# Performance work log

Measured on AMD Instinct MI355X. Metric: run time of the kernel, lower is better.

The kernel has to match this reference:

```python
import jax, jax.numpy as jnp
import numpy as np

B, T, F, C, D, R = 8, 1000, 96, 16, 64, 4
S = F // R
EPS = 1e-5


def _ln(x, g, b):
    # LayerNorm over last (frequency) dim, matching nn.LayerNorm(fe) on [B,C,T,F]
    m = jnp.mean(x, -1, keepdims=True)
    v = jnp.mean((x - m) ** 2, -1, keepdims=True)
    return (x - m) / jnp.sqrt(v + EPS) * g + b


def _gelu(x):
    return jax.nn.gelu(x, approximate=False)  # torch nn.GELU default (erf)


def setup_inputs() -> dict:
    key = jax.random.key(0)
    ks = jax.random.split(key, 16)
    def nrm(k, shape, fan_in):
        return jax.random.normal(k, shape, jnp.float32) / np.sqrt(fan_in)
    return {
        "input": jax.random.normal(ks[0], (B, 2, T, F), jnp.float32),
        "ln_in_g": jnp.ones((F,), jnp.float32),
        "ln_in_b": jnp.zeros((F,), jnp.float32),
        "w_in": nrm(ks[1], (C, 2), 2),
        "b_in": jnp.zeros((C,), jnp.float32),
        "gru_wx": nrm(ks[2], (3 * C, C), C),   # z|r|n input projections (1x1 conv, no bias)
        "gru_wh": nrm(ks[3], (3 * C, C), C),   # z|r|n hidden projections
        "ln_att_g": jnp.ones((F,), jnp.float32),
        "ln_att_b": jnp.zeros((F,), jnp.float32),
        "wq": nrm(ks[4], (D, C), C),
        "bq": jnp.zeros((D,), jnp.float32),
        "wk": nrm(ks[5], (D, C), C),
        "bk": jnp.zeros((D,), jnp.float32),
        "wv": nrm(ks[6], (D, C), C),
        "bv": jnp.zeros((D,), jnp.float32),
        "wo": nrm(ks[7], (C, D), D),
        "bo": jnp.zeros((C,), jnp.float32),
        "ln_m_g": jnp.ones((F,), jnp.float32),
        "ln_m_b": jnp.zeros((F,), jnp.float32),
        "w_m1": nrm(ks[8], (C, C), C),
        "b_m1": jnp.zeros((C,), jnp.float32),
        "w_m2": nrm(ks[9], (C, C), C),
        "b_m2": jnp.zeros((C,), jnp.float32),
        "ln_out_g": jnp.ones((F,), jnp.float32),
        "ln_out_b": jnp.zeros((F,), jnp.float32),
        "w_out": nrm(ks[10], (2, C), C),
        "b_out": jnp.zeros((2,), jnp.float32),
    }


def _fwd(input, ln_in_g, ln_in_b, w_in, b_in, gru_wx, gru_wh,
         ln_att_g, ln_att_b, wq, bq, wk, bk, wv, bv, wo, bo,
         ln_m_g, ln_m_b, w_m1, b_m1, w_m2, b_m2,
         ln_out_g, ln_out_b, w_out, b_out):
    b = input.shape[0]
    # conv_in: LayerNorm -> 1x1 Conv (2->C) -> GELU
    x = _gelu(jnp.einsum('oc,bctf->botf', w_in, _ln(input, ln_in_g, ln_in_b))
              + b_in[None, :, None, None])  # [B,C,T,F]

    # ConvGRU (kernel 1, no bias): precompute input gates, scan over time
    gx = jnp.einsum('gc,bctf->tbgf', gru_wx, x)  # [T,B,3C,F]
    h0 = jnp.zeros((b, C, F), x.dtype)

    def step(h, gx_t):
        gh = jnp.einsum('gc,bcf->bgf', gru_wh, h)
        zx, rx, nx = jnp.split(gx_t, 3, axis=1)
        zh, rh, nh = jnp.split(gh, 3, axis=1)
        z = jax.nn.sigmoid(zx + zh)
        r = jax.nn.sigmoid(rx + rh)
        n = jnp.tanh(nx + r * nh)
        h = (1.0 - z) * n + z * h
        return h, h

    h_last, hs = jax.lax.scan(step, h0, gx)
    x = x + jnp.moveaxis(hs, 0, 2)  # residual add of GRU output

    # PreNormShortcut(LongShortAttention): local window r + segment-pooled long keys over F
    y = _ln(x, ln_att_g, ln_att_b)
    q = jnp.einsum('dc,bctf->btfd', wq, y) + bq
    k = jnp.einsum('dc,bctf->btfd', wk, y) + bk
    v = jnp.einsum('dc,bctf->btfd', wv, y) + bv
    qs = q.reshape(b, T, S, R, D)
    kk = k.reshape(b, T, S, R, D)
    vv = v.reshape(b, T, S, R, D)
    k_long = kk.mean(3)  # [B,T,S,D]
    v_long = vv.mean(3)
    scale = D ** -0.5
    sc_s = jnp.einsum('btsqd,btskd->btsqk', qs, kk) * scale   # local scores [B,T,S,R,R]
    sc_l = jnp.einsum('btsqd,btmd->btsqm', qs, k_long) * scale  # long scores [B,T,S,R,S]
    a = jax.nn.softmax(jnp.concatenate([sc_s, sc_l], -1), axis=-1)
    o = (jnp.einsum('btsqk,btskd->btsqd', a[..., :R], vv)
         + jnp.einsum('btsqm,btmd->btsqd', a[..., R:], v_long))
    o = o.reshape(b, T, F, D)
    x = x + jnp.einsum('cd,btfd->bctf', wo, o) + bo[None, :, None, None]

    # PreNormShortcut(conv-GELU-conv)
    y = _ln(x, ln_m_g, ln_m_b)
    y = _gelu(jnp.einsum('oc,bctf->botf', w_m1, y) + b_m1[None, :, None, None])
    y = jnp.einsum('oc,bctf->botf', w_m2, y) + b_m2[None, :, None, None]
    x = x + y

    # conv_out: LayerNorm -> 1x1 Conv (C->2) -> Tanh, then outer residual
    y = jnp.tanh(jnp.einsum('oc,bctf->botf', w_out, _ln(x, ln_out_g, ln_out_b))
                 + b_out[None, :, None, None])
    return input + y, h_last


def reference(input, ln_in_g, ln_in_b, w_in, b_in, gru_wx, gru_wh,
              ln_att_g, ln_att_b, wq, bq, wk, bk, wv, bv, wo, bo,
              ln_m_g, ln_m_b, w_m1, b_m1, w_m2, b_m2,
              ln_out_g, ln_out_b, w_out, b_out):
    return _fwd(input, ln_in_g, ln_in_b, w_in, b_in, gru_wx, gru_wh,
                ln_att_g, ln_att_b, wq, bq, wk, bk, wv, bv, wo, bo,
                ln_m_g, ln_m_b, w_m1, b_m1, w_m2, b_m2,
                ln_out_g, ln_out_b, w_out, b_out)
```

## Files before the change

### kernel.cpp

```cpp
#include <hip/hip_runtime.h>
#include <math.h>

#define B_ 8
#define T_ 1000
#define F_ 96
#define C_ 16
#define D_ 64
#define EPS_ 1e-5f
#define CH_ 40

typedef short bfrag8 __attribute__((ext_vector_type(8)));
typedef float facc4 __attribute__((ext_vector_type(4)));
typedef float f2v __attribute__((ext_vector_type(2)));
#define MFMA16 __builtin_amdgcn_mfma_f32_16x16x32_bf16

__device__ __forceinline__ float gelu_erf(float v){
    return 0.5f*v*(1.0f+erff(v*0.70710678118654752440f));
}
__device__ __forceinline__ float dot4(float4 a, float4 b){
    return a.x*b.x + a.y*b.y + a.z*b.z + a.w*b.w;
}
__device__ __forceinline__ float ex2(float x){
    float r; asm("v_exp_f32 %0, %1" : "=v"(r) : "v"(x)); return r;
}
__device__ __forceinline__ float ex2n(float x){
    float r; asm("v_exp_f32 %0, -%1" : "=v"(r) : "v"(x)); return r;
}
__device__ __forceinline__ unsigned short f2bf(float x){
    unsigned int u = __float_as_uint(x);
    return (unsigned short)((u + 0x7fffu + ((u>>16)&1u)) >> 16);
}
__device__ __forceinline__ float bf2f(unsigned short s){
    return __uint_as_float(((unsigned int)s)<<16);
}
__device__ __forceinline__ unsigned int pack2bf(float a, float b){
    return (unsigned int)f2bf(a) | ((unsigned int)f2bf(b)<<16);
}

__global__ __launch_bounds__(256) void k_prep(
    const float* __restrict__ wq, const float* __restrict__ bq,
    const float* __restrict__ wk, const float* __restrict__ bk,
    const float* __restrict__ wv, const float* __restrict__ wo,
    const float* __restrict__ wm1, const float* __restrict__ wm2,
    short* __restrict__ gtb, float* __restrict__ uvw,
    short* __restrict__ wv_bf, short* __restrict__ wo_bf,
    short* __restrict__ wm1_bf, short* __restrict__ wm2_bf)
{
    int tid = threadIdx.x;
    int c1 = tid & 15, c2 = tid >> 4;
    float acc = 0.f;
    #pragma unroll 8
    for (int d=0; d<64; ++d)
        acc += wq[d*16 + c1] * wk[d*16 + c2];
    gtb[c2*16 + c1] = (short)f2bf(0.125f * acc);
    if (tid < 16){
        float a = 0.f;
        for (int d=0; d<64; ++d) a += wq[d*16 + tid] * bk[d];
        uvw[tid] = 0.125f * a;
    } else if (tid < 32){
        int cc = tid - 16;
        float a = 0.f;
        for (int d=0; d<64; ++d) a += bq[d] * wk[d*16 + cc];
        uvw[16 + cc] = 0.125f * a;
    } else if (tid == 32){
        float a = 0.f;
        for (int d=0; d<64; ++d) a += bq[d] * bk[d];
        uvw[32] = 0.125f * a;
    }
    for (int i = tid; i < 1024; i += 256){
        wv_bf[i] = (short)f2bf(wv[i]);
        wo_bf[i] = (short)f2bf(wo[i]);
    }
    if (tid < 256){
        wm1_bf[tid] = (short)f2bf(wm1[tid]);
        wm2_bf[tid] = (short)f2bf(wm2[tid]);
    }
}

__global__ __launch_bounds__(128) void k_conv_in(
    const float* __restrict__ in, const float* __restrict__ g, const float* __restrict__ bb,
    const float* __restrict__ w_in, const float* __restrict__ b_in,
    float* __restrict__ x)
{
    int bt = blockIdx.x; int b = bt / T_; int t = bt % T_;
    int tid = threadIdx.x;
    __shared__ float r0[128], r1[128], r2[128], r3[128];
    float i0=0.f, i1=0.f;
    size_t base0 = ((size_t)(b*2+0)*T_ + t)*F_;
    size_t base1 = ((size_t)(b*2+1)*T_ + t)*F_;
    if (tid < F_){ i0 = in[base0+tid]; i1 = in[base1+tid]; }
    r0[tid]=i0; r1[tid]=i0*i0; r2[tid]=i1; r3[tid]=i1*i1;
    __syncthreads();
    for (int s=64; s>0; s>>=1){
        if (tid < s){ r0[tid]+=r0[tid+s]; r1[tid]+=r1[tid+s]; r2[tid]+=r2[tid+s]; r3[tid]+=r3[tid+s]; }
        __syncthreads();
    }
    float m0 = r0[0]*(1.f/F_), m1 = r2[0]*(1.f/F_);
    float ri0 = rsqrtf(r1[0]*(1.f/F_) - m0*m0 + EPS_);
    float ri1 = rsqrtf(r3[0]*(1.f/F_) - m1*m1 + EPS_);
    if (tid < F_){
        float gg = g[tid], b0 = bb[tid];
        float y0 = (i0-m0)*ri0*gg + b0;
        float y1 = (i1-m1)*ri1*gg + b0;
        float xv[16];
        #pragma unroll
        for (int c=0;c<C_;++c){
            xv[c] = gelu_erf(w_in[c*2+0]*y0 + w_in[c*2+1]*y1 + b_in[c]);
        }
        float4* xp = (float4*)(x + (((size_t)b*T_+t)*F_ + tid)*C_);
        xp[0] = make_float4(xv[0],xv[1],xv[2],xv[3]);
        xp[1] = make_float4(xv[4],xv[5],xv[6],xv[7]);
        xp[2] = make_float4(xv[8],xv[9],xv[10],xv[11]);
        xp[3] = make_float4(xv[12],xv[13],xv[14],xv[15]);
    }
}

#define DPPF(src, ctrl) __int_as_float(__builtin_amdgcn_update_dpp(0, __float_as_int(src), (ctrl), 0xF, 0xF, false))
#define L2E_ 1.44269504088896340736f

__global__ __launch_bounds__(256, 1) void k_gru(
    const float* __restrict__ x, const float* __restrict__ wx, const float* __restrict__ wh,
    float* __restrict__ hs, float* __restrict__ d_out)
{
    int blk = blockIdx.x;
    int b = blk / 24, f0 = (blk % 24) * 4;
    int tid = threadIdx.x;
    int wave = tid >> 6, lane = tid & 63;
    int c = lane & 15, ch = lane >> 4;
    int f = f0 + ch;

    __shared__ float GG[2][(CH_+1)*192];

    if (wave != 0){
        float4 Wxz[4], Wxr[4], Wxn[4];
        #pragma unroll
        for (int q=0;q<4;++q){
            float4 az = *(const float4*)(wx + ( 0+c)*16 + 4*q);
            float4 ar = *(const float4*)(wx + (16+c)*16 + 4*q);
            float4 an = *(const float4*)(wx + (32+c)*16 + 4*q);
            Wxz[q] = make_float4(az.x*L2E_, az.y*L2E_, az.z*L2E_, az.w*L2E_);
            Wxr[q] = make_float4(ar.x*L2E_, ar.y*L2E_, ar.z*L2E_, ar.w*L2E_);
            Wxn[q] = make_float4(an.x*2.f*L2E_, an.y*2.f*L2E_, an.z*2.f*L2E_, an.w*2.f*L2E_);
        }
        const float* gb0 = x + (size_t)b*T_*(F_*C_) + f*C_;
        const int tl0 = (wave-1)*14;
        const int tl1 = (tl0 + 14 < CH_) ? tl0 + 14 : CH_;
        #define PRODUCE(K, BF) { \
            _Pragma("unroll 2") \
            for (int tl=tl0; tl<tl1; ++tl){ \
                const float* xp2 = gb0 + (size_t)((K)*CH_ + tl)*(F_*C_); \
                float4 x0 = *(const float4*)(xp2 + 0); \
                float4 x1 = *(const float4*)(xp2 + 4); \
                float4 x2 = *(const float4*)(xp2 + 8); \
                float4 x3 = *(const float4*)(xp2 + 12); \
                float zx = dot4(Wxz[0],x0)+dot4(Wxz[1],x1)+dot4(Wxz[2],x2)+dot4(Wxz[3],x3); \
                float rx = dot4(Wxr[0],x0)+dot4(Wxr[1],x1)+dot4(Wxr[2],x2)+dot4(Wxr[3],x3); \
                float nx = dot4(Wxn[0],x0)+dot4(Wxn[1],x1)+dot4(Wxn[2],x2)+dot4(Wxn[3],x3); \
                float* gq = &GG[BF][tl*192 + lane]; \
                gq[0] = zx; gq[64] = rx; gq[128] = nx; \
            } }
        PRODUCE(0, 0);
        __syncthreads();
        for (int k=0; k<T_/CH_; ++k){
            if (k+1 < T_/CH_){
                if ((k+1)&1){ PRODUCE(k+1, 1); } else { PRODUCE(k+1, 0); }
            }
            __syncthreads();
        }
        #undef PRODUCE
    } else {
        __builtin_amdgcn_s_setprio(1);
        const int pm0[8] = {0,2,7,5,15,13,8,10};
        const int pm1[8] = {1,3,6,4,14,12,9,11};
        f2v Wz[8], Wr[8], Wn[8];
        #pragma unroll
        for (int j=0;j<8;++j){
            int ka = c ^ pm0[j], kb = c ^ pm1[j];
            Wz[j].x = L2E_*wh[( 0+c)*16 + ka];      Wz[j].y = L2E_*wh[( 0+c)*16 + kb];
            Wr[j].x = L2E_*wh[(16+c)*16 + ka];      Wr[j].y = L2E_*wh[(16+c)*16 + kb];
            Wn[j].x = 2.f*L2E_*wh[(32+c)*16 + ka];  Wn[j].y = 2.f*L2E_*wh[(32+c)*16 + kb];
        }
        float hc = 0.f;
        size_t hsb = (size_t)b*T_*(F_*C_) + f0*C_ + lane;
        __syncthreads();
        for (int k=0; k<T_/CH_; ++k){
            const float* gp = GG[k&1];
            float gzv = gp[lane], grv = gp[64+lane], gnv = gp[128+lane];
            #pragma unroll 8
            for (int tl=0; tl<CH_; ++tl){
                const float* np = gp + (tl+1)*192 + lane;
                float gzn = np[0], grn = np[64], gnn = np[128];
                f2v A0, P2, P7, P5, PF, PD, P8, PA;
                A0.x = hc;              A0.y = DPPF(hc, 0xB1);
                P2.x = DPPF(A0.x,0x4E); P2.y = DPPF(A0.y,0x4E);
                P7.x = DPPF(A0.x,0x141);P7.y = DPPF(A0.y,0x141);
                P5.x = DPPF(P7.x,0x4E); P5.y = DPPF(P7.y,0x4E);
                PF.x = DPPF(A0.x,0x140);PF.y = DPPF(A0.y,0x140);
                PD.x = DPPF(PF.x,0x4E); PD.y = DPPF(PF.y,0x4E);
                P8.x = DPPF(PF.x,0x141);P8.y = DPPF(PF.y,0x141);
                PA.x = DPPF(P8.x,0x4E); PA.y = DPPF(P8.y,0x4E);
                f2v sz = Wz[0]*A0, sr = Wr[0]*A0, sn = Wn[0]*A0;
                sz = __builtin_elementwise_fma(Wz[1],P2,sz);
                sr = __builtin_elementwise_fma(Wr[1],P2,sr);
                sn = __builtin_elementwise_fma(Wn[1],P2,sn);
                sz = __builtin_elementwise_fma(Wz[2],P7,sz);
                sr = __builtin_elementwise_fma(Wr[2],P7,sr);
                sn = __builtin_elementwise_fma(Wn[2],P7,sn);
                sz = __builtin_elementwise_fma(Wz[3],P5,sz);
                sr = __builtin_elementwise_fma(Wr[3],P5,sr);
                sn = __builtin_elementwise_fma(Wn[3],P5,sn);
                sz = __builtin_elementwise_fma(Wz[4],PF,sz);
                sr = __builtin_elementwise_fma(Wr[4],PF,sr);
                sn = __builtin_elementwise_fma(Wn[4],PF,sn);
                sz = __builtin_elementwise_fma(Wz[5],PD,sz);
                sr = __builtin_elementwise_fma(Wr[5],PD,sr);
                sn = __builtin_elementwise_fma(Wn[5],PD,sn);
                sz = __builtin_elementwise_fma(Wz[6],P8,sz);
                sr = __builtin_elementwise_fma(Wr[6],P8,sr);
                sn = __builtin_elementwise_fma(Wn[6],P8,sn);
                sz = __builtin_elementwise_fma(Wz[7],PA,sz);
                sr = __builtin_elementwise_fma(Wr[7],PA,sr);
                sn = __builtin_elementwise_fma(Wn[7],PA,sn);
                float z = __builtin_amdgcn_rcpf(1.f + ex2n((gzv + sz.x) + sz.y));
                float r = __builtin_amdgcn_rcpf(1.f + ex2n((grv + sr.x) + sr.y));
                float u = __builtin_amdgcn_rcpf(1.f + ex2(fmaf(r, sn.x + sn.y, gnv)));
                float n = fmaf(-2.f, u, 1.f);
                hc = n + z*(hc - n);
                hs[hsb + (size_t)(k*CH_ + tl)*(F_*C_)] = hc;
                gzv = gzn; grv = grn; gnv = gnn;
            }
            __syncthreads();
        }
        d_out[(size_t)B_*2*T_*F_ + ((size_t)b*C_ + c)*F_ + f] = hc;
    }
}

#define XR_FL   0
#define YB_SH   3072
#define YGB_SH  5376
#define PG_SH   3072
#define YMB_SH  7680
#define E_FL    4224
#define GL_FL   4320
#define GM_FL   4416
#define VBT_SH  8880
#define VLBT_SH 15024
#define SC_FL   8536
#define OB_SH   17072
#define PL_SH   23216
#define GTB_SH  17072
#define UU_FL   8728
#define VV_FL   8744
#define W0_FL   8760
#define OSC_FL  8776
#define MEA_FL  9288
#define RST_FL  9304
#define TOTF    13144

__device__ __forceinline__ void ln_stats16(float* S, int tid){
    int c = tid & 15, g = tid >> 4;
    float s=0.f, q=0.f;
    #pragma unroll
    for (int i=0;i<6;++i){
        float v = S[XR_FL + (g*6+i)*16 + c];
        s += v; q += v*v;
    }
    S[OSC_FL + g*16 + c] = s;
    S[OSC_FL + 256 + g*16 + c] = q;
    __syncthreads();
    if (tid < 16){
        float Sm=0.f, Q=0.f;
        #pragma unroll
        for (int g2=0; g2<16; ++g2){
            Sm += S[OSC_FL + g2*16 + tid];
            Q  += S[OSC_FL + 256 + g2*16 + tid];
        }
        float m = Sm*(1.f/96.f);
        S[MEA_FL+tid] = m;
        S[RST_FL+tid] = rsqrtf(Q*(1.f/96.f) - m*m + EPS_);
    }
    __syncthreads();
}

__global__ __launch_bounds__(256) void k_tail(
    const float* __restrict__ x, const float* __restrict__ hs, const float* __restrict__ input,
    const float* __restrict__ ln_att_g, const float* __restrict__ ln_att_b,
    const short* __restrict__ gtb, const float* __restrict__ uvw,
    const short* __restrict__ wv_bf, const float* __restrict__ bv,
    const short* __restrict__ wo_bf, const float* __restrict__ bo,
    const float* __restrict__ ln_m_g, const float* __restrict__ ln_m_b,
    const short* __restrict__ wm1_bf, const float* __restrict__ bm1,
    const short* __restrict__ wm2_bf, const float* __restrict__ bm2,
    const float* __restrict__ ln_o_g, const float* __restrict__ ln_o_b,
    const float* __restrict__ w_out, const float* __restrict__ b_out,
    float* __restrict__ out)
{
    int bt = blockIdx.x; int b = bt / T_; int t = bt % T_;
    int tid = threadIdx.x;
    int w = tid >> 6, lane = tid & 63;
    int n = lane & 15, q2 = lane >> 4;
    __shared__ float S[TOTF];
    short* Ssh = (short*)S;
    const bfrag8 ZF = {0,0,0,0,0,0,0,0};
    const int svl = (n >> 1) & 3;
    const int swo = n & 7;

    size_t xbase = ((size_t)b*T_ + t)*(size_t)(F_*C_);

    {
        const float4* xg = (const float4*)(x + xbase);
        const float4* hg = (const float4*)(hs + xbase);
        float4* XR4 = (float4*)(S + XR_FL);
        for (int i4 = tid; i4 < 384; i4 += 256){
            float4 a = xg[i4], h = hg[i4];
            XR4[i4] = make_float4(a.x+h.x, a.y+h.y, a.z+h.z, a.w+h.w);
        }
        if (tid < 64){
            int cc2 = tid >> 2, c1g = (tid & 3)*4;
            *(uint2*)(Ssh + GTB_SH + cc2*24 + c1g) = *(const uint2*)(gtb + cc2*16 + c1g);
        } else if (tid < 97){
            S[UU_FL + (tid - 64)] = uvw[tid - 64];
        }
    }
    bfrag8 Bv = ZF, Bm1 = ZF, Bm2 = ZF;
    if (q2 < 2){
        Bv  = *(const bfrag8*)(wv_bf  + (16*w + n)*16 + q2*8);
        Bm1 = *(const bfrag8*)(wm1_bf + n*16 + q2*8);
        Bm2 = *(const bfrag8*)(wm2_bf + n*16 + q2*8);
    }
    bfrag8 Bo0 = *(const bfrag8*)(wo_bf + n*64 + q2*8);
    bfrag8 Bo1 = *(const bfrag8*)(wo_bf + n*64 + 32 + q2*8);
    float bvr  = bv[16*w + n];
    float bor  = bo[n];
    float bm1r = bm1[n];
    float bm2r = bm2[n];
    __syncthreads();

    ln_stats16(S, tid);

    {
        float4* XR4 = (float4*)(S + XR_FL);
        for (int i4 = tid; i4 < 384; i4 += 256){
            int f = i4 >> 2, c4 = i4 & 3;
            float4 v = XR4[i4];
            float4 m4 = *(float4*)(S + MEA_FL + 4*c4);
            float4 r4 = *(float4*)(S + RST_FL + 4*c4);
            float gg = ln_att_g[f], b2 = ln_att_b[f];
            float y0 = (v.x - m4.x)*r4.x*gg + b2;
            float y1 = (v.y - m4.y)*r4.y*gg + b2;
            float y2 = (v.z - m4.z)*r4.z*gg + b2;
            float y3 = (v.w - m4.w)*r4.w*gg + b2;
            uint2 pk = make_uint2(pack2bf(y0,y1), pack2bf(y2,y3));
            *(uint2*)(Ssh + YB_SH + f*24 + c4*4) = pk;
        }
    }
    __syncthreads();

    if (tid < 96){
        int f = tid;
        float yv[16];
        uint4 u0 = *(const uint4*)(Ssh + YB_SH + f*24);
        uint4 u1 = *(const uint4*)(Ssh + YB_SH + f*24 + 8);
        unsigned int uu[8] = {u0.x,u0.y,u0.z,u0.w,u1.x,u1.y,u1.z,u1.w};
        #pragma unroll
        for (int j=0;j<8;++j){
            yv[2*j]   = bf2f((unsigned short)(uu[j] & 0xffff));
            yv[2*j+1] = bf2f((unsigned short)(uu[j] >> 16));
        }
        float de = 0.f, dg = 0.f;
        #pragma unroll
        for (int cc=0; cc<16; ++cc){
            de += yv[cc]*S[UU_FL+cc];
            dg += yv[cc]*S[VV_FL+cc];
        }
        S[E_FL + f]  = de + S[W0_FL];
        S[GL_FL + f] = dg;
    }
    for (int e = tid; e < 384; e += 256){
        int m = e >> 4, cc = e & 15;
        float sm = bf2f((unsigned short)Ssh[YB_SH + (4*m+0)*24 + cc])
                 + bf2f((unsigned short)Ssh[YB_SH + (4*m+1)*24 + cc])
                 + bf2f((unsigned short)Ssh[YB_SH + (4*m+2)*24 + cc])
                 + bf2f((unsigned short)Ssh[YB_SH + (4*m+3)*24 + cc]);
        Ssh[YMB_SH + m*24 + cc] = (short)f2bf(0.25f*sm);
    }
    if (tid < 128){
        int row = 24 + (tid >> 4), cc = tid & 15;
        Ssh[YMB_SH + row*24 + cc] = 0;
    }
    __syncthreads();

    {
        #pragma unroll
        for (int mt=0; mt<6; ++mt){
            bfrag8 A = ZF;
            if (q2 < 2) A = *(const bfrag8*)(Ssh + YB_SH + (mt*16 + n)*24 + q2*8);
            facc4 acc = {bvr, bvr, bvr, bvr};
            acc = MFMA16(A, Bv, acc, 0, 0, 0);
            uint2 pk = make_uint2(pack2bf(acc[0],acc[1]), pack2bf(acc[2],acc[3]));
            int g = 2*mt + (q2>>1);
            *(uint2*)(Ssh + VBT_SH + (16*w + n)*96 + ((g^svl)<<3) + ((q2&1)<<2)) = pk;
        }
        #pragma unroll
        for (int mt=0; mt<2; ++mt){
            bfrag8 A = ZF;
            if (q2 < 2) A = *(const bfrag8*)(Ssh + YMB_SH + (mt*16 + n)*24 + q2*8);
            facc4 acc = {bvr, bvr, bvr, bvr};
            acc = MFMA16(A, Bv, acc, 0, 0, 0);
            uint2 pk = make_uint2(pack2bf(acc[0],acc[1]), pack2bf(acc[2],acc[3]));
            int g = 2*mt + (q2>>1);
            *(uint2*)(Ssh + VLBT_SH + (16*w + n)*32 + ((g^svl)<<3) + ((q2&1)<<2)) = pk;
        }
        bfrag8 Bg = ZF;
        if (q2 < 2) Bg = *(const bfrag8*)(Ssh + GTB_SH + n*24 + q2*8);
        for (int mt = w; mt < 6; mt += 4){
            bfrag8 A = ZF;
            if (q2 < 2) A = *(const bfrag8*)(Ssh + YB_SH + (mt*16 + n)*24 + q2*8);
            facc4 acc = {0.f,0.f,0.f,0.f};
            acc = MFMA16(A, Bg, acc, 0, 0, 0);
            #pragma unroll
            for (int r=0;r<4;++r)
                Ssh[YGB_SH + (mt*16 + q2*4 + r)*24 + n] = (short)f2bf(acc[r]);
        }
        if (tid >= 224 && tid < 248){
            int m = tid - 224;
            float a2 = 0.f;
            #pragma unroll
            for (int cc=0; cc<16; ++cc)
                a2 += bf2f((unsigned short)Ssh[YMB_SH + m*24 + cc]) * S[VV_FL + cc];
            S[GM_FL + m] = a2;
        }
    }
    __syncthreads();

    for (int j = w; j < 18; j += 4){
        int mt = j / 3, kind = j % 3;
        bfrag8 A = ZF;
        if (q2 < 2) A = *(const bfrag8*)(Ssh + YGB_SH + (mt*16 + n)*24 + q2*8);
        bfrag8 Bf = ZF;
        if (kind == 0){
            if (q2 < 2) Bf = *(const bfrag8*)(Ssh + YB_SH + (mt*16 + n)*24 + q2*8);
        } else {
            int nt = kind - 1;
            if (q2 < 2) Bf = *(const bfrag8*)(Ssh + YMB_SH + (nt*16 + n)*24 + q2*8);
        }
        facc4 acc = {0.f,0.f,0.f,0.f};
        acc = MFMA16(A, Bf, acc, 0, 0, 0);
        if (kind == 0){
            if ((n >> 2) == q2){
                #pragma unroll
                for (int r=0;r<4;++r)
                    S[SC_FL + (mt*16 + q2*4 + r)*29 + (n & 3)] = acc[r];
            }
        } else {
            int nt = kind - 1;
            if (!(nt == 1 && n >= 8)){
                #pragma unroll
                for (int r=0;r<4;++r)
                    S[SC_FL + (mt*16 + q2*4 + r)*29 + 4 + nt*16 + n] = acc[r];
            }
        }
    }
    __syncthreads();

    if (tid < 96){
        int f = tid;
        int lsq = (f >> 2) & 3;
        float e_ = S[E_FL + f];
        const float* row = S + SC_FL + f*29;
        float sl[4];
        #pragma unroll
        for (int j=0;j<4;++j)
            sl[j] = row[j] + e_ + S[GL_FL + (f & ~3) + j];
        float sg[24];
        #pragma unroll
        for (int m=0;m<24;++m)
            sg[m] = row[4 + m] + e_ + S[GM_FL + m];
        float mx = sl[0];
        #pragma unroll
        for (int j=1;j<4;++j) mx = fmaxf(mx, sl[j]);
        #pragma unroll
        for (int m=0;m<24;++m) mx = fmaxf(mx, sg[m]);
        float sum = 0.f;
        #pragma unroll
        for (int j=0;j<4;++j){ sl[j] = __expf(sl[j]-mx); sum += sl[j]; }
        #pragma unroll
        for (int m=0;m<24;++m){ sg[m] = __expf(sg[m]-mx); sum += sg[m]; }
        float inv = __builtin_amdgcn_rcpf(sum);
        unsigned int lo = pack2bf(sl[0]*inv, sl[1]*inv);
        unsigned int hi = pack2bf(sl[2]*inv, sl[3]*inv);
        uint4 z4 = make_uint4(0u,0u,0u,0u);
        uint4 p0 = make_uint4(lsq==0?lo:0u, lsq==0?hi:0u, lsq==1?lo:0u, lsq==1?hi:0u);
        uint4 p1 = make_uint4(lsq==2?lo:0u, lsq==2?hi:0u, lsq==3?lo:0u, lsq==3?hi:0u);
        uint4* plp = (uint4*)(Ssh + PL_SH + f*32);
        int swp = (f >> 1) & 3;
        plp[0^swp] = p0; plp[1^swp] = p1; plp[2^swp] = z4; plp[3^swp] = z4;
        unsigned int gdw[12];
        #pragma unroll
        for (int m=0;m<12;++m) gdw[m] = pack2bf(sg[2*m]*inv, sg[2*m+1]*inv);
        uint4* pgp = (uint4*)(Ssh + PG_SH + f*48);
        pgp[0] = make_uint4(gdw[0],gdw[1],gdw[2],gdw[3]);
        pgp[1] = make_uint4(gdw[4],gdw[5],gdw[6],gdw[7]);
        pgp[2] = make_uint4(gdw[8],gdw[9],gdw[10],gdw[11]);
        pgp[3] = z4;
    }
    __syncthreads();

    {
        bfrag8 Avl = *(const bfrag8*)(Ssh + VLBT_SH + (16*w + n)*32 + ((q2^svl)<<3));
        #pragma unroll
        for (int nt=0; nt<6; ++nt){
            bfrag8 Avb = *(const bfrag8*)(Ssh + VBT_SH + (16*w + n)*96 + (((2*nt + q2)^svl)<<3));
            bfrag8 Bpl = *(const bfrag8*)(Ssh + PL_SH + (nt*16 + n)*32 + ((q2^svl)<<3));
            bfrag8 Bpg = *(const bfrag8*)(Ssh + PG_SH + (nt*16 + n)*48 + q2*8);
            facc4 acc = {0.f,0.f,0.f,0.f};
            acc = MFMA16(Avb, Bpl, acc, 0, 0, 0);
            acc = MFMA16(Avl, Bpg, acc, 0, 0, 0);
            uint2 pk = make_uint2(pack2bf(acc[0],acc[1]), pack2bf(acc[2],acc[3]));
            int go = 2*w + (q2>>1);
            *(uint2*)(Ssh + OB_SH + (nt*16 + n)*64 + ((go^swo)<<3) + ((q2&1)<<2)) = pk;
        }
    }
    __syncthreads();

    for (int mt = w; mt < 6; mt += 4){
        bfrag8 A0 = *(const bfrag8*)(Ssh + OB_SH + (mt*16 + n)*64 + ((q2^swo)<<3));
        bfrag8 A1 = *(const bfrag8*)(Ssh + OB_SH + (mt*16 + n)*64 + (((4+q2)^swo)<<3));
        facc4 acc = {bor, bor, bor, bor};
        acc = MFMA16(A0, Bo0, acc, 0, 0, 0);
        acc = MFMA16(A1, Bo1, acc, 0, 0, 0);
        #pragma unroll
        for (int r=0;r<4;++r)
            S[XR_FL + (mt*16 + q2*4 + r)*16 + n] += acc[r];
    }
    __syncthreads();

    ln_stats16(S, tid);
    {
        float4* XR4 = (float4*)(S + XR_FL);
        for (int i4 = tid; i4 < 384; i4 += 256){
            int f = i4 >> 2, c4 = i4 & 3;
            float4 v = XR4[i4];
            float4 m4 = *(float4*)(S + MEA_FL + 4*c4);
            float4 r4 = *(float4*)(S + RST_FL + 4*c4);
            float gg = ln_m_g[f], b2 = ln_m_b[f];
            float y0 = (v.x - m4.x)*r4.x*gg + b2;
            float y1 = (v.y - m4.y)*r4.y*gg + b2;
            float y2 = (v.z - m4.z)*r4.z*gg + b2;
            float y3 = (v.w - m4.w)*r4.w*gg + b2;
            uint2 pk = make_uint2(pack2bf(y0,y1), pack2bf(y2,y3));
            *(uint2*)(Ssh + YB_SH + f*24 + c4*4) = pk;
        }
    }
    __syncthreads();
    for (int mt = w; mt < 6; mt += 4){
        bfrag8 A = ZF;
        if (q2 < 2) A = *(const bfrag8*)(Ssh + YB_SH + (mt*16 + n)*24 + q2*8);
        facc4 acc = {bm1r, bm1r, bm1r, bm1r};
        acc = MFMA16(A, Bm1, acc, 0, 0, 0);
        #pragma unroll
        for (int r=0;r<4;++r)
            Ssh[YGB_SH + (mt*16 + q2*4 + r)*24 + n] = (short)f2bf(gelu_erf(acc[r]));
    }
    __syncthreads();
    for (int mt = w; mt < 6; mt += 4){
        bfrag8 A = ZF;
        if (q2 < 2) A = *(const bfrag8*)(Ssh + YGB_SH + (mt*16 + n)*24 + q2*8);
        facc4 acc = {bm2r, bm2r, bm2r, bm2r};
        acc = MFMA16(A, Bm2, acc, 0, 0, 0);
        #pragma unroll
        for (int r=0;r<4;++r)
            S[XR_FL + (mt*16 + q2*4 + r)*16 + n] += acc[r];
    }
    __syncthreads();

    ln_stats16(S, tid);
    if (tid < 192){
        int ch = tid >= 96, f = tid - 96*ch;
        float gg = ln_o_g[f], b2 = ln_o_b[f];
        float acc = b_out[ch];
        float4* XR4 = (float4*)(S + XR_FL);
        #pragma unroll
        for (int c4=0;c4<4;++c4){
            float4 x4 = XR4[f*4 + c4];
            float4 m4 = *(float4*)(S + MEA_FL + 4*c4);
            float4 r4 = *(float4*)(S + RST_FL + 4*c4);
            float4 w4 = *(const float4*)(w_out + ch*16 + 4*c4);
            float4 tm;
            tm.x = (x4.x - m4.x)*r4.x*gg + b2;
            tm.y = (x4.y - m4.y)*r4.y*gg + b2;
            tm.z = (x4.z - m4.z)*r4.z*gg + b2;
            tm.w = (x4.w - m4.w)*r4.w*gg + b2;
            acc += dot4(w4, tm);
        }
        size_t oidx = ((size_t)(b*2+ch)*T_ + t)*F_ + f;
        out[oidx] = input[oidx] + tanhf(acc);
    }
}

extern "C" void kernel_launch(void* const* d_in, const int* in_sizes, int n_in,
                              void* d_out, int out_size, void* d_ws, size_t ws_size,
                              hipStream_t stream)
{
    const float* input   = (const float*)d_in[0];
    const float* ln_in_g = (const float*)d_in[1];
    const float* ln_in_b = (const float*)d_in[2];
    const float* w_in    = (const float*)d_in[3];
    const float* b_in    = (const float*)d_in[4];
    const float* gru_wx  = (const float*)d_in[5];
    const float* gru_wh  = (const float*)d_in[6];
    const float* ln_att_g= (const float*)d_in[7];
    const float* ln_att_b= (const float*)d_in[8];
    const float* wq = (const float*)d_in[9];
    const float* bq = (const float*)d_in[10];
    const float* wk = (const float*)d_in[11];
    const float* bk = (const float*)d_in[12];
    const float* wv = (const float*)d_in[13];
    const float* bv = (const float*)d_in[14];
    const float* wo = (const float*)d_in[15];
    const float* bo = (const float*)d_in[16];
    const float* ln_m_g = (const float*)d_in[17];
    const float* ln_m_b = (const float*)d_in[18];
    const float* w_m1 = (const float*)d_in[19];
    const float* b_m1 = (const float*)d_in[20];
    const float* w_m2 = (const float*)d_in[21];
    const float* b_m2 = (const float*)d_in[22];
    const float* ln_out_g = (const float*)d_in[23];
    const float* ln_out_b = (const float*)d_in[24];
    const float* w_out = (const float*)d_in[25];
    const float* b_out = (const float*)d_in[26];
    float* out = (float*)d_out;

    const size_t NX = (size_t)B_*T_*F_*C_;
    float* x   = (float*)d_ws;
    float* hs  = x + NX;
    float* uvw = x + 2*NX;
    short* wv_bf  = (short*)(x + 2*NX + 64);
    short* wo_bf  = wv_bf + 1024;
    short* wm1_bf = wo_bf + 1024;
    short* wm2_bf = wm1_bf + 256;
    short* gtb    = wm2_bf + 256;

    k_prep<<<1, 256, 0, stream>>>(wq, bq, wk, bk, wv, wo, w_m1, w_m2,
                                  gtb, uvw, wv_bf, wo_bf, wm1_bf, wm2_bf);
    k_conv_in<<<B_*T_, 128, 0, stream>>>(input, ln_in_g, ln_in_b, w_in, b_in, x);
    k_gru<<<192, 256, 0, stream>>>(x, gru_wx, gru_wh, hs, out);
    k_tail<<<B_*T_, 256, 0, stream>>>(x, hs, input, ln_att_g, ln_att_b,
        gtb, uvw, wv_bf, bv, wo_bf, bo, ln_m_g, ln_m_b, wm1_bf, b_m1, wm2_bf, b_m2,
        ln_out_g, ln_out_b, w_out, b_out, out);
}
```

Baseline: 419.1 us.

## Fuse conv_in into GRU producer waves with separate LayerNorm stats kernel

```diff
diff --git a/kernel.cpp b/kernel.cpp
--- a/kernel.cpp
+++ b/kernel.cpp
@@ -77,50 +77,76 @@
     }
 }
 
-__global__ __launch_bounds__(128) void k_conv_in(
-    const float* __restrict__ in, const float* __restrict__ g, const float* __restrict__ bb,
-    const float* __restrict__ w_in, const float* __restrict__ b_in,
-    float* __restrict__ x)
+__global__ __launch_bounds__(256) void k_stats(
+    const float* __restrict__ in, float* __restrict__ stats)
 {
-    int bt = blockIdx.x; int b = bt / T_; int t = bt % T_;
-    int tid = threadIdx.x;
-    __shared__ float r0[128], r1[128], r2[128], r3[128];
-    float i0=0.f, i1=0.f;
-    size_t base0 = ((size_t)(b*2+0)*T_ + t)*F_;
-    size_t base1 = ((size_t)(b*2+1)*T_ + t)*F_;
-    if (tid < F_){ i0 = in[base0+tid]; i1 = in[base1+tid]; }
-    r0[tid]=i0; r1[tid]=i0*i0; r2[tid]=i1; r3[tid]=i1*i1;
-    __syncthreads();
-    for (int s=64; s>0; s>>=1){
-        if (tid < s){ r0[tid]+=r0[tid+s]; r1[tid]+=r1[tid+s]; r2[tid]+=r2[tid+s]; r3[tid]+=r3[tid+s]; }
-        __syncthreads();
-    }
-    float m0 = r0[0]*(1.f/F_), m1 = r2[0]*(1.f/F_);
-    float ri0 = rsqrtf(r1[0]*(1.f/F_) - m0*m0 + EPS_);
-    float ri1 = rsqrtf(r3[0]*(1.f/F_) - m1*m1 + EPS_);
-    if (tid < F_){
-        float gg = g[tid], b0 = bb[tid];
-        float y0 = (i0-m0)*ri0*gg + b0;
-        float y1 = (i1-m1)*ri1*gg + b0;
-        float xv[16];
-        #pragma unroll
-        for (int c=0;c<C_;++c){
-            xv[c] = gelu_erf(w_in[c*2+0]*y0 + w_in[c*2+1]*y1 + b_in[c]);
-        }
-        float4* xp = (float4*)(x + (((size_t)b*T_+t)*F_ + tid)*C_);
-        xp[0] = make_float4(xv[0],xv[1],xv[2],xv[3]);
-        xp[1] = make_float4(xv[4],xv[5],xv[6],xv[7]);
-        xp[2] = make_float4(xv[8],xv[9],xv[10],xv[11]);
-        xp[3] = make_float4(xv[12],xv[13],xv[14],xv[15]);
+    int row = blockIdx.x*8 + (threadIdx.x>>5);
+    int l32 = threadIdx.x & 31;
+    const float* rp = in + (size_t)row*F_;
+    float s = 0.f, q = 0.f;
+    #pragma unroll
+    for (int j=0;j<3;++j){
+        float v = rp[l32 + 32*j];
+        s += v; q += v*v;
+    }
+    #pragma unroll
+    for (int o=16;o>0;o>>=1){
+        s += __shfl_xor(s, o, 32);
+        q += __shfl_xor(q, o, 32);
+    }
+    if (l32 == 0){
+        int b = row / (2*T_);
+        int rem = row % (2*T_);
+        int chn = rem / T_, t = rem % T_;
+        float m = s*(1.f/F_);
+        float ri = rsqrtf(q*(1.f/F_) - m*m + EPS_);
+        float* sp = stats + ((size_t)(b*T_ + t))*4 + chn*2;
+        sp[0] = m; sp[1] = ri;
     }
 }
 
 #define DPPF(src, ctrl) __int_as_float(__builtin_amdgcn_update_dpp(0, __float_as_int(src), (ctrl), 0xF, 0xF, false))
 #define L2E_ 1.44269504088896340736f
 
+#define GATHER_PAIRDOTS(XV, WZ, WR, WN, SZ, SR, SN) { \
+    f2v A0,P2,P7,P5,PF,PD,P8,PA; \
+    A0.x = (XV);            A0.y = DPPF((XV),0xB1); \
+    P2.x = DPPF(A0.x,0x4E); P2.y = DPPF(A0.y,0x4E); \
+    P7.x = DPPF(A0.x,0x141);P7.y = DPPF(A0.y,0x141); \
+    P5.x = DPPF(P7.x,0x4E); P5.y = DPPF(P7.y,0x4E); \
+    PF.x = DPPF(A0.x,0x140);PF.y = DPPF(A0.y,0x140); \
+    PD.x = DPPF(PF.x,0x4E); PD.y = DPPF(PF.y,0x4E); \
+    P8.x = DPPF(PF.x,0x141);P8.y = DPPF(PF.y,0x141); \
+    PA.x = DPPF(P8.x,0x4E); PA.y = DPPF(P8.y,0x4E); \
+    f2v sza = WZ[0]*A0, sra = WR[0]*A0, sna = WN[0]*A0; \
+    sza = __builtin_elementwise_fma(WZ[1],P2,sza); \
+    sra = __builtin_elementwise_fma(WR[1],P2,sra); \
+    sna = __builtin_elementwise_fma(WN[1],P2,sna); \
+    sza = __builtin_elementwise_fma(WZ[2],P7,sza); \
+    sra = __builtin_elementwise_fma(WR[2],P7,sra); \
+    sna = __builtin_elementwise_fma(WN[2],P7,sna); \
+    sza = __builtin_elementwise_fma(WZ[3],P5,sza); \
+    sra = __builtin_elementwise_fma(WR[3],P5,sra); \
+    sna = __builtin_elementwise_fma(WN[3],P5,sna); \
+    f2v szb = WZ[4]*PF, srb = WR[4]*PF, snb = WN[4]*PF; \
+    szb = __builtin_elementwise_fma(WZ[5],PD,szb); \
+    srb = __builtin_elementwise_fma(WR[5],PD,srb); \
+    snb = __builtin_elementwise_fma(WN[5],PD,snb); \
+    szb = __builtin_elementwise_fma(WZ[6],P8,szb); \
+    srb = __builtin_elementwise_fma(WR[6],P8,srb); \
+    snb = __builtin_elementwise_fma(WN[6],P8,snb); \
+    szb = __builtin_elementwise_fma(WZ[7],PA,szb); \
+    srb = __builtin_elementwise_fma(WR[7],PA,srb); \
+    snb = __builtin_elementwise_fma(WN[7],PA,snb); \
+    SZ = sza + szb; SR = sra + srb; SN = sna + snb; \
+}
+
 __global__ __launch_bounds__(256, 1) void k_gru(
-    const float* __restrict__ x, const float* __restrict__ wx, const float* __restrict__ wh,
-    float* __restrict__ hs, float* __restrict__ d_out)
+    const float* __restrict__ input, const float* __restrict__ stats,
+    const float* __restrict__ ln_in_g, const float* __restrict__ ln_in_b,
+    const float* __restrict__ w_in, const float* __restrict__ b_in,
+    const float* __restrict__ wx, const float* __restrict__ wh,
+    float* __restrict__ x, float* __restrict__ hs, float* __restrict__ d_out)
 {
     int blk = blockIdx.x;
     int b = blk / 24, f0 = (blk % 24) * 4;
@@ -131,33 +157,41 @@
 
     __shared__ float GG[2][(CH_+1)*192];
 
+    const int pm0[8] = {0,2,7,5,15,13,8,10};
+    const int pm1[8] = {1,3,6,4,14,12,9,11};
+
     if (wave != 0){
-        float4 Wxz[4], Wxr[4], Wxn[4];
-        #pragma unroll
-        for (int q=0;q<4;++q){
-            float4 az = *(const float4*)(wx + ( 0+c)*16 + 4*q);
-            float4 ar = *(const float4*)(wx + (16+c)*16 + 4*q);
-            float4 an = *(const float4*)(wx + (32+c)*16 + 4*q);
-            Wxz[q] = make_float4(az.x*L2E_, az.y*L2E_, az.z*L2E_, az.w*L2E_);
-            Wxr[q] = make_float4(ar.x*L2E_, ar.y*L2E_, ar.z*L2E_, ar.w*L2E_);
-            Wxn[q] = make_float4(an.x*2.f*L2E_, an.y*2.f*L2E_, an.z*2.f*L2E_, an.w*2.f*L2E_);
-        }
-        const float* gb0 = x + (size_t)b*T_*(F_*C_) + f*C_;
+        f2v Xz[8], Xr[8], Xn[8];
+        #pragma unroll
+        for (int j=0;j<8;++j){
+            int ka = c ^ pm0[j], kb = c ^ pm1[j];
+            Xz[j].x = L2E_*wx[( 0+c)*16 + ka];      Xz[j].y = L2E_*wx[( 0+c)*16 + kb];
+            Xr[j].x = L2E_*wx[(16+c)*16 + ka];      Xr[j].y = L2E_*wx[(16+c)*16 + kb];
+            Xn[j].x = 2.f*L2E_*wx[(32+c)*16 + ka];  Xn[j].y = 2.f*L2E_*wx[(32+c)*16 + kb];
+        }
+        float wi0 = w_in[c*2+0], wi1 = w_in[c*2+1], biv = b_in[c];
+        float gf = ln_in_g[f], bfv = ln_in_b[f];
+        const float* in0p = input + (size_t)(b*2+0)*T_*F_;
+        const float* in1p = input + (size_t)(b*2+1)*T_*F_;
+        const float4* stats4 = (const float4*)stats;
+        float* xout = x + (size_t)b*T_*(F_*C_) + f0*C_;
         const int tl0 = (wave-1)*14;
         const int tl1 = (tl0 + 14 < CH_) ? tl0 + 14 : CH_;
         #define PRODUCE(K, BF) { \
             _Pragma("unroll 2") \
             for (int tl=tl0; tl<tl1; ++tl){ \
-                const float* xp2 = gb0 + (size_t)((K)*CH_ + tl)*(F_*C_); \
-                float4 x0 = *(const float4*)(xp2 + 0); \
-                float4 x1 = *(const float4*)(xp2 + 4); \
-                float4 x2 = *(const float4*)(xp2 + 8); \
-                float4 x3 = *(const float4*)(xp2 + 12); \
-                float zx = dot4(Wxz[0],x0)+dot4(Wxz[1],x1)+dot4(Wxz[2],x2)+dot4(Wxz[3],x3); \
-                float rx = dot4(Wxr[0],x0)+dot4(Wxr[1],x1)+dot4(Wxr[2],x2)+dot4(Wxr[3],x3); \
-                float nx = dot4(Wxn[0],x0)+dot4(Wxn[1],x1)+dot4(Wxn[2],x2)+dot4(Wxn[3],x3); \
+                int tt = (K)*CH_ + tl; \
+                float i0 = in0p[(size_t)tt*F_ + f]; \
+                float i1 = in1p[(size_t)tt*F_ + f]; \
+                float4 st = stats4[(size_t)b*T_ + tt]; \
+                float y0 = (i0 - st.x)*st.y*gf + bfv; \
+                float y1 = (i1 - st.z)*st.w*gf + bfv; \
+                float xv = gelu_erf(wi0*y0 + wi1*y1 + biv); \
+                xout[(size_t)tt*(F_*C_) + lane] = xv; \
+                f2v SZ, SR, SN; \
+                GATHER_PAIRDOTS(xv, Xz, Xr, Xn, SZ, SR, SN); \
                 float* gq = &GG[BF][tl*192 + lane]; \
-                gq[0] = zx; gq[64] = rx; gq[128] = nx; \
+                gq[0] = SZ.x + SZ.y; gq[64] = SR.x + SR.y; gq[128] = SN.x + SN.y; \
             } }
         PRODUCE(0, 0);
         __syncthreads();
@@ -170,8 +204,6 @@
         #undef PRODUCE
     } else {
         __builtin_amdgcn_s_setprio(1);
-        const int pm0[8] = {0,2,7,5,15,13,8,10};
-        const int pm1[8] = {1,3,6,4,14,12,9,11};
         f2v Wz[8], Wr[8], Wn[8];
         #pragma unroll
         for (int j=0;j<8;++j){
@@ -190,40 +222,11 @@
             for (int tl=0; tl<CH_; ++tl){
                 const float* np = gp + (tl+1)*192 + lane;
                 float gzn = np[0], grn = np[64], gnn = np[128];
-                f2v A0, P2, P7, P5, PF, PD, P8, PA;
-                A0.x = hc;              A0.y = DPPF(hc, 0xB1);
-                P2.x = DPPF(A0.x,0x4E); P2.y = DPPF(A0.y,0x4E);
-                P7.x = DPPF(A0.x,0x141);P7.y = DPPF(A0.y,0x141);
-                P5.x = DPPF(P7.x,0x4E); P5.y = DPPF(P7.y,0x4E);
-                PF.x = DPPF(A0.x,0x140);PF.y = DPPF(A0.y,0x140);
-                PD.x = DPPF(PF.x,0x4E); PD.y = DPPF(PF.y,0x4E);
-                P8.x = DPPF(PF.x,0x141);P8.y = DPPF(PF.y,0x141);
-                PA.x = DPPF(P8.x,0x4E); PA.y = DPPF(P8.y,0x4E);
-                f2v sz = Wz[0]*A0, sr = Wr[0]*A0, sn = Wn[0]*A0;
-                sz = __builtin_elementwise_fma(Wz[1],P2,sz);
-                sr = __builtin_elementwise_fma(Wr[1],P2,sr);
-                sn = __builtin_elementwise_fma(Wn[1],P2,sn);
-                sz = __builtin_elementwise_fma(Wz[2],P7,sz);
-                sr = __builtin_elementwise_fma(Wr[2],P7,sr);
-                sn = __builtin_elementwise_fma(Wn[2],P7,sn);
-                sz = __builtin_elementwise_fma(Wz[3],P5,sz);
-                sr = __builtin_elementwise_fma(Wr[3],P5,sr);
-                sn = __builtin_elementwise_fma(Wn[3],P5,sn);
-                sz = __builtin_elementwise_fma(Wz[4],PF,sz);
-                sr = __builtin_elementwise_fma(Wr[4],PF,sr);
-                sn = __builtin_elementwise_fma(Wn[4],PF,sn);
-                sz = __builtin_elementwise_fma(Wz[5],PD,sz);
-                sr = __builtin_elementwise_fma(Wr[5],PD,sr);
-                sn = __builtin_elementwise_fma(Wn[5],PD,sn);
-                sz = __builtin_elementwise_fma(Wz[6],P8,sz);
-                sr = __builtin_elementwise_fma(Wr[6],P8,sr);
-                sn = __builtin_elementwise_fma(Wn[6],P8,sn);
-                sz = __builtin_elementwise_fma(Wz[7],PA,sz);
-                sr = __builtin_elementwise_fma(Wr[7],PA,sr);
-                sn = __builtin_elementwise_fma(Wn[7],PA,sn);
-                float z = __builtin_amdgcn_rcpf(1.f + ex2n((gzv + sz.x) + sz.y));
-                float r = __builtin_amdgcn_rcpf(1.f + ex2n((grv + sr.x) + sr.y));
-                float u = __builtin_amdgcn_rcpf(1.f + ex2(fmaf(r, sn.x + sn.y, gnv)));
+                f2v SZ, SR, SN;
+                GATHER_PAIRDOTS(hc, Wz, Wr, Wn, SZ, SR, SN);
+                float z = __builtin_amdgcn_rcpf(1.f + ex2n(gzv + (SZ.x + SZ.y)));
+                float r = __builtin_amdgcn_rcpf(1.f + ex2n(grv + (SR.x + SR.y)));
+                float u = __builtin_amdgcn_rcpf(1.f + ex2(fmaf(r, SN.x + SN.y, gnv)));
                 float n = fmaf(-2.f, u, 1.f);
                 hc = n + z*(hc - n);
                 hs[hsb + (size_t)(k*CH_ + tl)*(F_*C_)] = hc;
@@ -640,11 +643,13 @@
     short* wm1_bf = wo_bf + 1024;
     short* wm2_bf = wm1_bf + 256;
     short* gtb    = wm2_bf + 256;
+    float* stats = out;
 
     k_prep<<<1, 256, 0, stream>>>(wq, bq, wk, bk, wv, wo, w_m1, w_m2,
                                   gtb, uvw, wv_bf, wo_bf, wm1_bf, wm2_bf);
-    k_conv_in<<<B_*T_, 128, 0, stream>>>(input, ln_in_g, ln_in_b, w_in, b_in, x);
-    k_gru<<<192, 256, 0, stream>>>(x, gru_wx, gru_wh, hs, out);
+    k_stats<<<B_*2*T_/8, 256, 0, stream>>>(input, stats);
+    k_gru<<<192, 256, 0, stream>>>(input, stats, ln_in_g, ln_in_b, w_in, b_in,
+                                   gru_wx, gru_wh, x, hs, out);
     k_tail<<<B_*T_, 256, 0, stream>>>(x, hs, input, ln_att_g, ln_att_b,
         gtb, uvw, wv_bf, bv, wo_bf, bo, ln_m_g, ln_m_b, wm1_bf, b_m1, wm2_bf, b_m2,
         ln_out_g, ln_out_b, w_out, b_out, out);
```

Measured after the change: 423.7 us. About the same (+1.1%).
